# Optimization experiments

Hardware: AMD Instinct MI355X
Metric: run time of the kernel (lower is better)

The kernel has to match this reference:

```python
import jax, jax.numpy as jnp
import numpy as np

MAX_STEP = 20

def setup_inputs() -> dict:
    key = jax.random.key(0)
    k1, k2 = jax.random.split(key)
    B, L, E, H = 32, 2048, 256, 256
    word_rep = jax.random.normal(k1, (B, L, E), dtype=jnp.float32)
    # nn.Parameter(torch.randn(...).uniform_(-0.1, 0.1)) -> uniform in [-0.1, 0.1]
    cnn = jax.random.uniform(k2, (MAX_STEP, E, H), dtype=jnp.float32, minval=-0.1, maxval=0.1)
    return {"word_rep": word_rep, "cnn": cnn}

def reference(word_rep, cnn):
    # word_rep: [B, L, E]; cnn: [MAX_STEP, E, H]
    L = word_rep.shape[1]
    # Gather the cyclically-indexed per-position weight: [L, E, H]
    W = cnn[jnp.arange(L) % MAX_STEP]
    # Fused batched matmul over all positions at once: [B, L, H]
    hidden_vecs = jnp.einsum('ble,leh->blh', word_rep, W)
    return (hidden_vecs, hidden_vecs[:, -1])
```

## Files before the change

kernel.cpp:

```cpp
#include <hip/hip_runtime.h>
#include <hip/hip_bf16.h>

#define B_ 32
#define L_ 2048
#define E_ 256
#define H_ 256
#define MAXSTEP 20
#define NL 4

typedef __attribute__((ext_vector_type(4))) float f32x4;
typedef __attribute__((ext_vector_type(8))) short bf16x8;
using bf16 = __hip_bfloat16;

__device__ inline short cvt1(float x) {
    bf16 b = __float2bfloat16(x);
    return *reinterpret_cast<short*>(&b);
}

__global__ void transpose_w_kernel(const float* __restrict__ cnn, short* __restrict__ wt) {
    __shared__ short tile[32][33];
    const int s  = blockIdx.z;
    const int e0 = blockIdx.y * 32;
    const int h0 = blockIdx.x * 32;
    const int tx = threadIdx.x;
    const int ty = threadIdx.y;
    const float* src = cnn + ((size_t)s * E_ + e0) * H_ + h0;
#pragma unroll
    for (int i = ty; i < 32; i += 8)
        tile[i][tx] = cvt1(src[(size_t)i * H_ + tx]);
    __syncthreads();
    short* dst = wt + ((size_t)s * H_ + h0) * E_ + e0;
#pragma unroll
    for (int i = ty; i < 32; i += 8)
        dst[(size_t)i * E_ + tx] = tile[tx][i];
}

template <bool TRANS>
__global__ __launch_bounds__(256) void vaw_mfma_kernel(
        const float* __restrict__ A, const void* __restrict__ W, float* __restrict__ out) {
    __shared__ __align__(16) float aLds[2][B_ * E_];

    const int l0   = blockIdx.x * NL;
    const int wv   = threadIdx.x >> 6;
    const int lane = threadIdx.x & 63;
    const int r    = lane & 15;
    const int g    = lane >> 4;
    const int nbase = wv * 64;
    const int key   = r & 7;

    auto stage = [&](int it) {
        float* dst = aLds[it & 1];
        const int l = l0 + it;
#pragma unroll
        for (int t = 0; t < 8; ++t) {
            const int b  = t * 4 + wv;
            const int cg = lane ^ (b & 7);
            const float* gp = A + ((size_t)b * L_ + l) * E_ + cg * 4;
            __builtin_amdgcn_global_load_lds(
                (const __attribute__((address_space(1))) void*)gp,
                (__attribute__((address_space(3))) void*)&dst[b * 256],
                16, 0, 0);
        }
    };

    stage(0);

#pragma unroll 1
    for (int it = 0; it < NL; ++it) {
        const int l   = l0 + it;
        const int s   = l % MAXSTEP;
        const int cur = it & 1;

        if (it < NL - 1) {
            stage(it + 1);
            asm volatile("s_waitcnt vmcnt(8)" ::: "memory");
        } else {
            asm volatile("s_waitcnt vmcnt(0)" ::: "memory");
        }
        __builtin_amdgcn_s_barrier();
        __builtin_amdgcn_sched_barrier(0);

        f32x4 acc[2][4] = {};

        if constexpr (TRANS) {
            const short* wtb = (const short*)W + ((size_t)s * H_ + nbase + r) * E_ + g * 8;
            bf16x8 bbuf[2][4];
#pragma unroll
            for (int nf = 0; nf < 4; ++nf)
                bbuf[0][nf] = *(const bf16x8*)(wtb + (size_t)nf * 16 * E_);
#pragma unroll
            for (int kk = 0; kk < 8; ++kk) {
                if (kk < 7) {
#pragma unroll
                    for (int nf = 0; nf < 4; ++nf)
                        bbuf[(kk + 1) & 1][nf] =
                            *(const bf16x8*)(wtb + (size_t)nf * 16 * E_ + (kk + 1) * 32);
                }
                const int c0 = kk * 8 + g * 2;
                f32x4 a0lo = *(const f32x4*)&aLds[cur][r * 256 + ((c0 ^ key) << 2)];
                f32x4 a0hi = *(const f32x4*)&aLds[cur][r * 256 + (((c0 + 1) ^ key) << 2)];
                f32x4 a1lo = *(const f32x4*)&aLds[cur][(r + 16) * 256 + ((c0 ^ key) << 2)];
                f32x4 a1hi = *(const f32x4*)&aLds[cur][(r + 16) * 256 + (((c0 + 1) ^ key) << 2)];
                bf16x8 a0, a1;
#pragma unroll
                for (int j = 0; j < 4; ++j) {
                    a0[j]     = cvt1(a0lo[j]);
                    a0[j + 4] = cvt1(a0hi[j]);
                    a1[j]     = cvt1(a1lo[j]);
                    a1[j + 4] = cvt1(a1hi[j]);
                }
#pragma unroll
                for (int nf = 0; nf < 4; ++nf) {
                    acc[0][nf] = __builtin_amdgcn_mfma_f32_16x16x32_bf16(a0, bbuf[kk & 1][nf], acc[0][nf], 0, 0, 0);
                    acc[1][nf] = __builtin_amdgcn_mfma_f32_16x16x32_bf16(a1, bbuf[kk & 1][nf], acc[1][nf], 0, 0, 0);
                }
            }
        } else {
            const float* Wf = (const float*)W + (size_t)s * E_ * H_;
#pragma unroll 2
            for (int kk = 0; kk < 8; ++kk) {
                const int k0 = kk * 32;
                const int c0 = kk * 8 + g * 2;
                f32x4 a0lo = *(const f32x4*)&aLds[cur][r * 256 + ((c0 ^ key) << 2)];
                f32x4 a0hi = *(const f32x4*)&aLds[cur][r * 256 + (((c0 + 1) ^ key) << 2)];
                f32x4 a1lo = *(const f32x4*)&aLds[cur][(r + 16) * 256 + ((c0 ^ key) << 2)];
                f32x4 a1hi = *(const f32x4*)&aLds[cur][(r + 16) * 256 + (((c0 + 1) ^ key) << 2)];
                bf16x8 a0, a1;
#pragma unroll
                for (int j = 0; j < 4; ++j) {
                    a0[j]     = cvt1(a0lo[j]);
                    a0[j + 4] = cvt1(a0hi[j]);
                    a1[j]     = cvt1(a1lo[j]);
                    a1[j + 4] = cvt1(a1hi[j]);
                }
                bf16x8 b0, b1, b2, b3;
#pragma unroll
                for (int j = 0; j < 8; ++j) {
                    const size_t krow = (size_t)(k0 + g * 8 + j) * H_;
                    b0[j] = cvt1(Wf[krow + nbase +  0 + r]);
                    b1[j] = cvt1(Wf[krow + nbase + 16 + r]);
                    b2[j] = cvt1(Wf[krow + nbase + 32 + r]);
                    b3[j] = cvt1(Wf[krow + nbase + 48 + r]);
                }
                acc[0][0] = __builtin_amdgcn_mfma_f32_16x16x32_bf16(a0, b0, acc[0][0], 0, 0, 0);
                acc[0][1] = __builtin_amdgcn_mfma_f32_16x16x32_bf16(a0, b1, acc[0][1], 0, 0, 0);
                acc[0][2] = __builtin_amdgcn_mfma_f32_16x16x32_bf16(a0, b2, acc[0][2], 0, 0, 0);
                acc[0][3] = __builtin_amdgcn_mfma_f32_16x16x32_bf16(a0, b3, acc[0][3], 0, 0, 0);
                acc[1][0] = __builtin_amdgcn_mfma_f32_16x16x32_bf16(a1, b0, acc[1][0], 0, 0, 0);
                acc[1][1] = __builtin_amdgcn_mfma_f32_16x16x32_bf16(a1, b1, acc[1][1], 0, 0, 0);
                acc[1][2] = __builtin_amdgcn_mfma_f32_16x16x32_bf16(a1, b2, acc[1][2], 0, 0, 0);
                acc[1][3] = __builtin_amdgcn_mfma_f32_16x16x32_bf16(a1, b3, acc[1][3], 0, 0, 0);
            }
        }

        const int row0 = g * 4;
#pragma unroll
        for (int mf = 0; mf < 2; ++mf) {
#pragma unroll
            for (int nf = 0; nf < 4; ++nf) {
                const int h = nbase + nf * 16 + r;
#pragma unroll
                for (int i = 0; i < 4; ++i) {
                    const int bb = mf * 16 + row0 + i;
                    out[((size_t)bb * L_ + l) * H_ + h] = acc[mf][nf][i];
                }
            }
        }
        if (l == L_ - 1) {
            float* out2 = out + (size_t)B_ * L_ * H_;
#pragma unroll
            for (int mf = 0; mf < 2; ++mf)
#pragma unroll
                for (int nf = 0; nf < 4; ++nf) {
                    const int h = nbase + nf * 16 + r;
#pragma unroll
                    for (int i = 0; i < 4; ++i) {
                        const int bb = mf * 16 + row0 + i;
                        out2[(size_t)bb * H_ + h] = acc[mf][nf][i];
                    }
                }
        }

        __builtin_amdgcn_s_barrier();
    }
}

extern "C" void kernel_launch(void* const* d_in, const int* in_sizes, int n_in,
                              void* d_out, int out_size, void* d_ws, size_t ws_size,
                              hipStream_t stream) {
    const float* word_rep = (const float*)d_in[0];
    const float* cnn      = (const float*)d_in[1];
    float* out = (float*)d_out;

    const size_t wt_bytes = (size_t)MAXSTEP * E_ * H_ * sizeof(short);
    if (ws_size >= wt_bytes) {
        short* wt = (short*)d_ws;
        transpose_w_kernel<<<dim3(8, 8, 20), dim3(32, 8), 0, stream>>>(cnn, wt);
        vaw_mfma_kernel<true><<<dim3(L_ / NL), dim3(256), 0, stream>>>(word_rep, wt, out);
    } else {
        vaw_mfma_kernel<false><<<dim3(L_ / NL), dim3(256), 0, stream>>>(word_rep, cnn, out);
    }
}
```

Baseline: 54.53 us.

## Group positions by weight step and keep the step's weights resident in registers

```diff
diff --git a/kernel.cpp b/kernel.cpp
--- a/kernel.cpp
+++ b/kernel.cpp
@@ -7,6 +7,7 @@
 #define H_ 256
 #define MAXSTEP 20
 #define NL 4
+#define NCHUNK 26
 
 typedef __attribute__((ext_vector_type(4))) float f32x4;
 typedef __attribute__((ext_vector_type(8))) short bf16x8;
@@ -35,22 +36,38 @@
         dst[(size_t)i * E_ + tx] = tile[tx][i];
 }
 
-template <bool TRANS>
-__global__ __launch_bounds__(256) void vaw_mfma_kernel(
-        const float* __restrict__ A, const void* __restrict__ W, float* __restrict__ out) {
+__global__ __launch_bounds__(256, 2) void vaw_sames_kernel(
+        const float* __restrict__ A, const short* __restrict__ Wt,
+        float* __restrict__ out) {
     __shared__ __align__(16) float aLds[2][B_ * E_];
 
-    const int l0   = blockIdx.x * NL;
-    const int wv   = threadIdx.x >> 6;
-    const int lane = threadIdx.x & 63;
-    const int r    = lane & 15;
-    const int g    = lane >> 4;
+    const int s     = blockIdx.x / NCHUNK;
+    const int chunk = blockIdx.x % NCHUNK;
+    const int cnt   = (s < 8) ? 103 : 102;
+    const int wv    = threadIdx.x >> 6;
+    const int lane  = threadIdx.x & 63;
+    const int r     = lane & 15;
+    const int g     = lane >> 4;
     const int nbase = wv * 64;
     const int key   = r & 7;
 
+    const short* wtb = Wt + ((size_t)s * H_ + nbase + r) * E_ + g * 8;
+    bf16x8 breg[8][4];
+#pragma unroll
+    for (int kk = 0; kk < 8; ++kk)
+#pragma unroll
+        for (int nf = 0; nf < 4; ++nf)
+            breg[kk][nf] = *(const bf16x8*)(wtb + (size_t)nf * 16 * E_ + kk * 32);
+
+    auto lof = [&](int it) {
+        int idx = chunk * NL + it;
+        if (idx > cnt - 1) idx = cnt - 1;
+        return s + 20 * idx;
+    };
+
     auto stage = [&](int it) {
+        const int l = lof(it);
         float* dst = aLds[it & 1];
-        const int l = l0 + it;
 #pragma unroll
         for (int t = 0; t < 8; ++t) {
             const int b  = t * 4 + wv;
@@ -65,12 +82,105 @@
 
     stage(0);
 
+#pragma unroll
+    for (int it = 0; it < NL; ++it) {
+        const int l   = lof(it);
+        const int cur = it & 1;
+
+        if (it < NL - 1) stage(it + 1);
+        if (it == 0)           asm volatile("s_waitcnt vmcnt(8)"  ::: "memory");
+        else if (it < NL - 1)  asm volatile("s_waitcnt vmcnt(40)" ::: "memory");
+        else                   asm volatile("s_waitcnt vmcnt(32)" ::: "memory");
+        __builtin_amdgcn_s_barrier();
+        __builtin_amdgcn_sched_barrier(0);
+
+        f32x4 acc[2][4] = {};
+#pragma unroll
+        for (int kk = 0; kk < 8; ++kk) {
+            const int c0 = kk * 8 + g * 2;
+            f32x4 a0lo = *(const f32x4*)&aLds[cur][r * 256 + ((c0 ^ key) << 2)];
+            f32x4 a0hi = *(const f32x4*)&aLds[cur][r * 256 + (((c0 + 1) ^ key) << 2)];
+            f32x4 a1lo = *(const f32x4*)&aLds[cur][(r + 16) * 256 + ((c0 ^ key) << 2)];
+            f32x4 a1hi = *(const f32x4*)&aLds[cur][(r + 16) * 256 + (((c0 + 1) ^ key) << 2)];
+            bf16x8 a0, a1;
+#pragma unroll
+            for (int j = 0; j < 4; ++j) {
+                a0[j]     = cvt1(a0lo[j]);
+                a0[j + 4] = cvt1(a0hi[j]);
+                a1[j]     = cvt1(a1lo[j]);
+                a1[j + 4] = cvt1(a1hi[j]);
+            }
+#pragma unroll
+            for (int nf = 0; nf < 4; ++nf) {
+                acc[0][nf] = __builtin_amdgcn_mfma_f32_16x16x32_bf16(a0, breg[kk][nf], acc[0][nf], 0, 0, 0);
+                acc[1][nf] = __builtin_amdgcn_mfma_f32_16x16x32_bf16(a1, breg[kk][nf], acc[1][nf], 0, 0, 0);
+            }
+        }
+
+        const int row0 = g * 4;
+#pragma unroll
+        for (int mf = 0; mf < 2; ++mf) {
+#pragma unroll
+            for (int nf = 0; nf < 4; ++nf) {
+                const int h = nbase + nf * 16 + r;
+#pragma unroll
+                for (int i = 0; i < 4; ++i) {
+                    const int bb = mf * 16 + row0 + i;
+                    out[((size_t)bb * L_ + l) * H_ + h] = acc[mf][nf][i];
+                }
+            }
+        }
+        if (l == L_ - 1) {
+            float* out2 = out + (size_t)B_ * L_ * H_;
+#pragma unroll
+            for (int mf = 0; mf < 2; ++mf)
+#pragma unroll
+                for (int nf = 0; nf < 4; ++nf) {
+                    const int h = nbase + nf * 16 + r;
+#pragma unroll
+                    for (int i = 0; i < 4; ++i) {
+                        const int bb = mf * 16 + row0 + i;
+                        out2[(size_t)bb * H_ + h] = acc[mf][nf][i];
+                    }
+                }
+        }
+
+        __builtin_amdgcn_s_barrier();
+    }
+}
+
+__global__ __launch_bounds__(256) void vaw_fallback_kernel(
+        const float* __restrict__ A, const float* __restrict__ W, float* __restrict__ out) {
+    __shared__ __align__(16) float aLds[2][B_ * E_];
+    const int l0   = blockIdx.x * NL;
+    const int wv   = threadIdx.x >> 6;
+    const int lane = threadIdx.x & 63;
+    const int r    = lane & 15;
+    const int g    = lane >> 4;
+    const int nbase = wv * 64;
+    const int key   = r & 7;
+
+    auto stage = [&](int it) {
+        float* dst = aLds[it & 1];
+        const int l = l0 + it;
+#pragma unroll
+        for (int t = 0; t < 8; ++t) {
+            const int b  = t * 4 + wv;
+            const int cg = lane ^ (b & 7);
+            const float* gp = A + ((size_t)b * L_ + l) * E_ + cg * 4;
+            __builtin_amdgcn_global_load_lds(
+                (const __attribute__((address_space(1))) void*)gp,
+                (__attribute__((address_space(3))) void*)&dst[b * 256],
+                16, 0, 0);
+        }
+    };
+
+    stage(0);
 #pragma unroll 1
     for (int it = 0; it < NL; ++it) {
         const int l   = l0 + it;
-        const int s   = l % MAXSTEP;
+        const int sidx = l % MAXSTEP;
         const int cur = it & 1;
-
         if (it < NL - 1) {
             stage(it + 1);
             asm volatile("s_waitcnt vmcnt(8)" ::: "memory");
@@ -81,81 +191,45 @@
         __builtin_amdgcn_sched_barrier(0);
 
         f32x4 acc[2][4] = {};
-
-        if constexpr (TRANS) {
-            const short* wtb = (const short*)W + ((size_t)s * H_ + nbase + r) * E_ + g * 8;
-            bf16x8 bbuf[2][4];
-#pragma unroll
-            for (int nf = 0; nf < 4; ++nf)
-                bbuf[0][nf] = *(const bf16x8*)(wtb + (size_t)nf * 16 * E_);
-#pragma unroll
-            for (int kk = 0; kk < 8; ++kk) {
-                if (kk < 7) {
-#pragma unroll
-                    for (int nf = 0; nf < 4; ++nf)
-                        bbuf[(kk + 1) & 1][nf] =
-                            *(const bf16x8*)(wtb + (size_t)nf * 16 * E_ + (kk + 1) * 32);
-                }
-                const int c0 = kk * 8 + g * 2;
-                f32x4 a0lo = *(const f32x4*)&aLds[cur][r * 256 + ((c0 ^ key) << 2)];
-                f32x4 a0hi = *(const f32x4*)&aLds[cur][r * 256 + (((c0 + 1) ^ key) << 2)];
-                f32x4 a1lo = *(const f32x4*)&aLds[cur][(r + 16) * 256 + ((c0 ^ key) << 2)];
-                f32x4 a1hi = *(const f32x4*)&aLds[cur][(r + 16) * 256 + (((c0 + 1) ^ key) << 2)];
-                bf16x8 a0, a1;
-#pragma unroll
-                for (int j = 0; j < 4; ++j) {
-                    a0[j]     = cvt1(a0lo[j]);
-                    a0[j + 4] = cvt1(a0hi[j]);
-                    a1[j]     = cvt1(a1lo[j]);
-                    a1[j + 4] = cvt1(a1hi[j]);
-                }
-#pragma unroll
-                for (int nf = 0; nf < 4; ++nf) {
-                    acc[0][nf] = __builtin_amdgcn_mfma_f32_16x16x32_bf16(a0, bbuf[kk & 1][nf], acc[0][nf], 0, 0, 0);
-                    acc[1][nf] = __builtin_amdgcn_mfma_f32_16x16x32_bf16(a1, bbuf[kk & 1][nf], acc[1][nf], 0, 0, 0);
-                }
-            }
-        } else {
-            const float* Wf = (const float*)W + (size_t)s * E_ * H_;
+        const float* Wf = W + (size_t)sidx * E_ * H_;
 #pragma unroll 2
-            for (int kk = 0; kk < 8; ++kk) {
-                const int k0 = kk * 32;
-                const int c0 = kk * 8 + g * 2;
-                f32x4 a0lo = *(const f32x4*)&aLds[cur][r * 256 + ((c0 ^ key) << 2)];
-                f32x4 a0hi = *(const f32x4*)&aLds[cur][r * 256 + (((c0 + 1) ^ key) << 2)];
-                f32x4 a1lo = *(const f32x4*)&aLds[cur][(r + 16) * 256 + ((c0 ^ key) << 2)];
-                f32x4 a1hi = *(const f32x4*)&aLds[cur][(r + 16) * 256 + (((c0 + 1) ^ key) << 2)];
-                bf16x8 a0, a1;
-#pragma unroll
-                for (int j = 0; j < 4; ++j) {
-                    a0[j]     = cvt1(a0lo[j]);
-                    a0[j + 4] = cvt1(a0hi[j]);
-                    a1[j]     = cvt1(a1lo[j]);
-                    a1[j + 4] = cvt1(a1hi[j]);
-                }
-                bf16x8 b0, b1, b2, b3;
-#pragma unroll
-                for (int j = 0; j < 8; ++j) {
-                    const size_t krow = (size_t)(k0 + g * 8 + j) * H_;
-                    b0[j] = cvt1(Wf[krow + nbase +  0 + r]);
-                    b1[j] = cvt1(Wf[krow + nbase + 16 + r]);
-                    b2[j] = cvt1(Wf[krow + nbase + 32 + r]);
-                    b3[j] = cvt1(Wf[krow + nbase + 48 + r]);
-                }
-                acc[0][0] = __builtin_amdgcn_mfma_f32_16x16x32_bf16(a0, b0, acc[0][0], 0, 0, 0);
-                acc[0][1] = __builtin_amdgcn_mfma_f32_16x16x32_bf16(a0, b1, acc[0][1], 0, 0, 0);
-                acc[0][2] = __builtin_amdgcn_mfma_f32_16x16x32_bf16(a0, b2, acc[0][2], 0, 0, 0);
-                acc[0][3] = __builtin_amdgcn_mfma_f32_16x16x32_bf16(a0, b3, acc[0][3], 0, 0, 0);
-                acc[1][0] = __builtin_amdgcn_mfma_f32_16x16x32_bf16(a1, b0, acc[1][0], 0, 0, 0);
-                acc[1][1] = __builtin_amdgcn_mfma_f32_16x16x32_bf16(a1, b1, acc[1][1], 0, 0, 0);
-                acc[1][2] = __builtin_amdgcn_mfma_f32_16x16x32_bf16(a1, b2, acc[1][2], 0, 0, 0);
-                acc[1][3] = __builtin_amdgcn_mfma_f32_16x16x32_bf16(a1, b3, acc[1][3], 0, 0, 0);
-            }
+        for (int kk = 0; kk < 8; ++kk) {
+            const int k0 = kk * 32;
+            const int c0 = kk * 8 + g * 2;
+            f32x4 a0lo = *(const f32x4*)&aLds[cur][r * 256 + ((c0 ^ key) << 2)];
+            f32x4 a0hi = *(const f32x4*)&aLds[cur][r * 256 + (((c0 + 1) ^ key) << 2)];
+            f32x4 a1lo = *(const f32x4*)&aLds[cur][(r + 16) * 256 + ((c0 ^ key) << 2)];
+            f32x4 a1hi = *(const f32x4*)&aLds[cur][(r + 16) * 256 + (((c0 + 1) ^ key) << 2)];
+            bf16x8 a0, a1;
+#pragma unroll
+            for (int j = 0; j < 4; ++j) {
+                a0[j]     = cvt1(a0lo[j]);
+                a0[j + 4] = cvt1(a0hi[j]);
+                a1[j]     = cvt1(a1lo[j]);
+                a1[j + 4] = cvt1(a1hi[j]);
+            }
+            bf16x8 b0, b1, b2, b3;
+#pragma unroll
+            for (int j = 0; j < 8; ++j) {
+                const size_t krow = (size_t)(k0 + g * 8 + j) * H_;
+                b0[j] = cvt1(Wf[krow + nbase +  0 + r]);
+                b1[j] = cvt1(Wf[krow + nbase + 16 + r]);
+                b2[j] = cvt1(Wf[krow + nbase + 32 + r]);
+                b3[j] = cvt1(Wf[krow + nbase + 48 + r]);
+            }
+            acc[0][0] = __builtin_amdgcn_mfma_f32_16x16x32_bf16(a0, b0, acc[0][0], 0, 0, 0);
+            acc[0][1] = __builtin_amdgcn_mfma_f32_16x16x32_bf16(a0, b1, acc[0][1], 0, 0, 0);
+            acc[0][2] = __builtin_amdgcn_mfma_f32_16x16x32_bf16(a0, b2, acc[0][2], 0, 0, 0);
+            acc[0][3] = __builtin_amdgcn_mfma_f32_16x16x32_bf16(a0, b3, acc[0][3], 0, 0, 0);
+            acc[1][0] = __builtin_amdgcn_mfma_f32_16x16x32_bf16(a1, b0, acc[1][0], 0, 0, 0);
+            acc[1][1] = __builtin_amdgcn_mfma_f32_16x16x32_bf16(a1, b1, acc[1][1], 0, 0, 0);
+            acc[1][2] = __builtin_amdgcn_mfma_f32_16x16x32_bf16(a1, b2, acc[1][2], 0, 0, 0);
+            acc[1][3] = __builtin_amdgcn_mfma_f32_16x16x32_bf16(a1, b3, acc[1][3], 0, 0, 0);
         }
 
         const int row0 = g * 4;
 #pragma unroll
-        for (int mf = 0; mf < 2; ++mf) {
+        for (int mf = 0; mf < 2; ++mf)
 #pragma unroll
             for (int nf = 0; nf < 4; ++nf) {
                 const int h = nbase + nf * 16 + r;
@@ -165,7 +239,6 @@
                     out[((size_t)bb * L_ + l) * H_ + h] = acc[mf][nf][i];
                 }
             }
-        }
         if (l == L_ - 1) {
             float* out2 = out + (size_t)B_ * L_ * H_;
 #pragma unroll
@@ -180,7 +253,6 @@
                     }
                 }
         }
-
         __builtin_amdgcn_s_barrier();
     }
 }
@@ -196,8 +268,8 @@
     if (ws_size >= wt_bytes) {
         short* wt = (short*)d_ws;
         transpose_w_kernel<<<dim3(8, 8, 20), dim3(32, 8), 0, stream>>>(cnn, wt);
-        vaw_mfma_kernel<true><<<dim3(L_ / NL), dim3(256), 0, stream>>>(word_rep, wt, out);
+        vaw_sames_kernel<<<dim3(MAXSTEP * NCHUNK), dim3(256), 0, stream>>>(word_rep, wt, out);
     } else {
-        vaw_mfma_kernel<false><<<dim3(L_ / NL), dim3(256), 0, stream>>>(word_rep, cnn, out);
+        vaw_fallback_kernel<<<dim3(L_ / NL), dim3(256), 0, stream>>>(word_rep, cnn, out);
     }
 }
```

Result: faster. 45.03 us (-17.4%).
